# Kernel tuning notes

Hardware: AMD Instinct MI355X
Metric: run time of the kernel (lower is better)

Reference implementation:

```python
import jax, jax.numpy as jnp
import numpy as np


def setup_inputs() -> dict:
    key = jax.random.key(0)
    ks = jax.random.split(key, 5)
    B, C, H, W = 4, 256, 64, 64
    C8 = C // 8
    x = jax.random.normal(ks[0], (B, C, H, W), dtype=jnp.float32)
    # conv1x1 weights stored as [out, in] (kernel size 1 squeezed)
    wq = jax.random.normal(ks[1], (C8, C), dtype=jnp.float32) * (1.0 / np.sqrt(C))
    wk = jax.random.normal(ks[2], (C8, C), dtype=jnp.float32) * (1.0 / np.sqrt(C))
    wv = jax.random.normal(ks[3], (C, C), dtype=jnp.float32) * (1.0 / np.sqrt(C))
    bq = jnp.zeros((C8,), dtype=jnp.float32)
    bk = jnp.zeros((C8,), dtype=jnp.float32)
    bv = jnp.zeros((C,), dtype=jnp.float32)
    gamma = jax.random.normal(ks[4], (1,), dtype=jnp.float32)
    return {"x": x, "wq": wq, "bq": bq, "wk": wk, "bk": bk, "wv": wv, "bv": bv, "gamma": gamma}


def reference(x, wq, bq, wk, bk, wv, bv, gamma):
    B, C, H, W = x.shape
    flat = x.reshape(B, C, H * W)                      # [B, C, N]
    # 1x1 conv == channel matmul
    q = jnp.einsum('oc,bcn->bon', wq, flat) + bq[:, None]   # [B, C/8, N]
    k = jnp.einsum('oc,bcn->bon', wk, flat) + bk[:, None]   # [B, C/8, N]
    v = jnp.einsum('oc,bcn->bon', wv, flat) + bv[:, None]   # [B, C, N]
    # query permuted to [B, N, C/8]; scores [B, N, N]
    qk = jnp.einsum('bcn,bcm->bnm', q, k)
    # NOTE: softmax over dim=1 (over query index n), matching torch softmax(qk, 1)
    attn = jax.nn.softmax(qk, axis=1)
    out_attn = jnp.einsum('bcn,bnm->bcm', v, attn)     # [B, C, N]
    out = gamma[0] * out_attn.reshape(B, C, H, W) + x
    return out
```

## Files before the change

### kernel.cpp

```cpp
#include <hip/hip_runtime.h>

#define Bsz 4
#define Cch 256
#define Nsp 4096
#define XT_STRIDE 264

typedef _Float16 half8 __attribute__((ext_vector_type(8)));
typedef _Float16 half4v __attribute__((ext_vector_type(4)));
typedef short short8_t __attribute__((ext_vector_type(8)));
typedef float f32x4 __attribute__((ext_vector_type(4)));
typedef float fl4 __attribute__((ext_vector_type(4)));
typedef unsigned short ushort4v __attribute__((ext_vector_type(4)));

static __device__ __forceinline__ unsigned short f2bf(float f) {
  unsigned u = __builtin_bit_cast(unsigned, f);
  u += 0x7FFFu + ((u >> 16) & 1u);
  return (unsigned short)(u >> 16);
}

__global__ __launch_bounds__(256) void wconv_kernel(
    const float* __restrict__ wq, const float* __restrict__ wk, const float* __restrict__ wv,
    const float* __restrict__ bq, const float* __restrict__ bk, const float* __restrict__ bv,
    _Float16* __restrict__ Wh, float* __restrict__ bias)
{
  int t = blockIdx.x * 256 + threadIdx.x;
  int idx0 = t * 4;
  int o = idx0 >> 8, c = idx0 & 255;
  const float* src = (o < 32) ? (wq + o * 256)
                   : (o < 64) ? (wk + (o - 32) * 256)
                              : (wv + (o - 64) * 256);
  fl4 w4 = *(const fl4*)(src + c);
  half4v h;
#pragma unroll
  for (int j = 0; j < 4; ++j) h[j] = (_Float16)w4[j];
  *(half4v*)(Wh + idx0) = h;
  if (t < 320) bias[t] = (t < 32) ? bq[t] : (t < 64) ? bk[t - 32] : bv[t - 64];
}

__global__ __launch_bounds__(256) void proj_kernel(
    const float* __restrict__ x, const _Float16* __restrict__ Wh,
    const float* __restrict__ bias,
    _Float16* __restrict__ qh, _Float16* __restrict__ kh,
    unsigned short* __restrict__ vbuf)
{
  int bid = blockIdx.x;
  int nt  = bid & 127;
  int b   = bid >> 7;
  int n0  = nt * 32;
  int tid = threadIdx.x;
  int w   = tid >> 6, lane = tid & 63;
  int l15 = lane & 15, lg = lane >> 4;

  __shared__ __align__(16) _Float16 xT[32 * XT_STRIDE];

  const float* xb = x + (size_t)b * Cch * Nsp;

  {
    int n = lane & 31, ch = lane >> 5;
#pragma unroll
    for (int i = 0; i < 4; ++i) {
      int c0 = i * 64 + w * 16 + ch * 8;
      half8 hv;
#pragma unroll
      for (int j = 0; j < 8; ++j)
        hv[j] = (_Float16)xb[(size_t)(c0 + j) * Nsp + n0 + n];
      *(half8*)&xT[n * XT_STRIDE + c0] = hv;
    }
  }
  __syncthreads();

  int nsub = (w & 1) * 16;
  half8 bX[8];
#pragma unroll
  for (int k = 0; k < 8; ++k)
    bX[k] = *(const half8*)&xT[(nsub + l15) * XT_STRIDE + k * 32 + lg * 8];

  int n = n0 + nsub + l15;
  int ot0 = (w >> 1) * 10;
#pragma unroll
  for (int t = 0; t < 10; ++t) {
    int ot = ot0 + t;
    const _Float16* wrow = Wh + (size_t)(ot * 16 + l15) * 256 + lg * 8;
    f32x4 acc; acc[0]=0.f; acc[1]=0.f; acc[2]=0.f; acc[3]=0.f;
#pragma unroll
    for (int k = 0; k < 8; ++k) {
      half8 aW = *(const half8*)(wrow + k * 32);
      acc = __builtin_amdgcn_mfma_f32_16x16x32_f16(aW, bX[k], acc, 0, 0, 0);
    }
    fl4 bs = *(const fl4*)(bias + ot * 16 + lg * 4);
    if (ot < 2) {
      half4v qv;
#pragma unroll
      for (int r = 0; r < 4; ++r) qv[r] = (_Float16)(acc[r] + bs[r]);
      *(half4v*)(qh + ((size_t)b * Nsp + n) * 32 + ot * 16 + lg * 4) = qv;
    } else if (ot < 4) {
      half4v kv;
#pragma unroll
      for (int r = 0; r < 4; ++r) kv[r] = (_Float16)(acc[r] + bs[r]);
      *(half4v*)(kh + ((size_t)b * Nsp + n) * 32 + (ot - 2) * 16 + lg * 4) = kv;
    } else {
      int cv = (ot - 4) * 16 + lg * 4;
#pragma unroll
      for (int r = 0; r < 4; ++r)
        vbuf[((size_t)b * Cch + cv + r) * Nsp + n] = f2bf(acc[r] + bs[r]);
    }
  }
}

__global__ __launch_bounds__(1024) void attn_kernel(
    const _Float16* __restrict__ qh, const _Float16* __restrict__ kh,
    const unsigned short* __restrict__ vb, const float* __restrict__ x,
    const float* __restrict__ gamma, float* __restrict__ out)
{
  int bid  = blockIdx.x;
  int xcd  = bid & 7;
  int slot = bid >> 3;
  int b    = xcd >> 1;
  int mt   = slot + 32 * (xcd & 1);
  int m0   = mt * 64;
  int tid  = threadIdx.x;
  int w    = tid >> 6;
  int lane = tid & 63;
  int l15  = lane & 15, lg = lane >> 4;
  int wk   = w >> 3, wc = w & 7;

  __shared__ __align__(16) unsigned short P_lds[2][64][256];
  __shared__ float dpart[16][64];
  __shared__ float denom_s[64];

  const _Float16*       qb    = qh + (size_t)b * Nsp * 32;
  const _Float16*       kb    = kh + (size_t)b * Nsp * 32;
  const unsigned short* vbase = vb + (size_t)b * Cch * Nsp;

  half8 kB[4];
#pragma unroll
  for (int j = 0; j < 4; ++j)
    kB[j] = *(const half8*)(kb + (size_t)(m0 + 16 * j + l15) * 32 + lg * 8);

  f32x4 acc[2][4];
#pragma unroll
  for (int i = 0; i < 2; ++i)
#pragma unroll
    for (int j = 0; j < 4; ++j) { acc[i][j][0]=0.f; acc[i][j][1]=0.f; acc[i][j][2]=0.f; acc[i][j][3]=0.f; }

  float dsum[4] = {0.f, 0.f, 0.f, 0.f};

  const _Float16*       qp  = qb + (size_t)(16 * w + l15) * 32 + lg * 8;
  const unsigned short* pv0 = vbase + (size_t)(32 * wc + l15) * Nsp + 128 * wk + lg * 8;
  const unsigned short* pv1 = pv0 + (size_t)16 * Nsp;
  int xorh  = 8 * (l15 & 7);
  int wcol  = (16 * w + 4 * lg) ^ xorh;
  int rbase = 128 * wk + 8 * lg;

  half8 qA_a, qA_b;
  qA_a = *(const half8*)qp;

#define BODY(IT, BUF, QCUR, QNXT)                                              \
  {                                                                            \
    int n0 = (IT) * 256;                                                       \
    short8_t vf[4][2];  \
    _Pragma("unroll")                                                          \
    for (int k = 0; k < 4; ++k) {                                              \
      vf[k][0] = *(const short8_t*)(pv0 + n0 + 32 * k);                        \
      vf[k][1] = *(const short8_t*)(pv1 + n0 + 32 * k);                        \
    }                                                                          \
    f32x4 S[4];                                                                \
    _Pragma("unroll")                                                          \
    for (int j = 0; j < 4; ++j) {                                              \
      f32x4 z; z[0]=0.f; z[1]=0.f; z[2]=0.f; z[3]=0.f;                         \
      S[j] = __builtin_amdgcn_mfma_f32_16x16x32_f16(QCUR, kB[j], z, 0, 0, 0);  \
    }                                                                          \
    QNXT = *(const half8*)(qp + (size_t)(((IT) + 1) & 15) * 8192);             \
    ushort4v pb[4];                                                            \
    _Pragma("unroll")                                                          \
    for (int j = 0; j < 4; ++j) {                                              \
      _Pragma("unroll")                                                        \
      for (int r = 0; r < 4; ++r) {                                            \
        float p = __expf(S[j][r] - 20.0f);                                     \
        dsum[j] += p;                                                          \
        pb[j][r] = f2bf(p);                                                    \
      }                                                                        \
    }                                                                          \
    _Pragma("unroll")                                                          \
    for (int j = 0; j < 4; ++j)                                                \
      *(ushort4v*)&P_lds[BUF][16 * j + l15][wcol] = pb[j];                     \
    __syncthreads();                                                           \
    __builtin_amdgcn_s_setprio(1);                                             \
    _Pragma("unroll")                                                          \
    for (int k = 0; k < 4; ++k) {                                              \
      _Pragma("unroll")                                                        \
      for (int j = 0; j < 4; ++j) {                                            \
        int rc = (rbase + 32 * k) ^ xorh;                                      \
        short8_t bP = *(const short8_t*)&P_lds[BUF][16 * j + l15][rc];         \
        acc[0][j] = __builtin_amdgcn_mfma_f32_16x16x32_bf16(vf[k][0], bP, acc[0][j], 0, 0, 0); \
        acc[1][j] = __builtin_amdgcn_mfma_f32_16x16x32_bf16(vf[k][1], bP, acc[1][j], 0, 0, 0); \
      }                                                                        \
    }                                                                          \
    __builtin_amdgcn_s_setprio(0);                                             \
  }

  for (int it = 0; it < 16; it += 2) {
    BODY(it,     0, qA_a, qA_b)
    BODY(it + 1, 1, qA_b, qA_a)
  }
#undef BODY

#pragma unroll
  for (int j = 0; j < 4; ++j) {
    float d = dsum[j];
    d += __shfl_xor(d, 16);
    d += __shfl_xor(d, 32);
    dsum[j] = d;
  }
  if (lane < 16) {
#pragma unroll
    for (int j = 0; j < 4; ++j) dpart[w][16 * j + lane] = dsum[j];
  }
  __syncthreads();
  if (tid < 64) {
    float s = 0.f;
#pragma unroll
    for (int ww = 0; ww < 16; ++ww) s += dpart[ww][tid];
    denom_s[tid] = s;
  }
  float* mbuf = (float*)P_lds;
  if (w >= 8) {
#pragma unroll
    for (int c16 = 0; c16 < 2; ++c16)
#pragma unroll
      for (int j = 0; j < 4; ++j)
#pragma unroll
        for (int r = 0; r < 4; ++r)
          mbuf[lane + 64 * (((c16 * 4 + j) * 4 + r) + 32 * (w - 8))] = acc[c16][j][r];
  }
  __syncthreads();
  if (w < 8) {
    float g = gamma[0];
#pragma unroll
    for (int c16 = 0; c16 < 2; ++c16) {
#pragma unroll
      for (int j = 0; j < 4; ++j) {
        float dn = denom_s[16 * j + l15];
#pragma unroll
        for (int r = 0; r < 4; ++r) {
          float a = acc[c16][j][r] + mbuf[lane + 64 * (((c16 * 4 + j) * 4 + r) + 32 * w)];
          int c = 32 * w + 16 * c16 + 4 * lg + r;
          int m = m0 + 16 * j + l15;
          size_t idx = ((size_t)b * Cch + c) * Nsp + m;
          out[idx] = g * (a / dn) + x[idx];
        }
      }
    }
  }
}

extern "C" void kernel_launch(void* const* d_in, const int* in_sizes, int n_in,
                              void* d_out, int out_size, void* d_ws, size_t ws_size,
                              hipStream_t stream) {
  const float* x     = (const float*)d_in[0];
  const float* wq    = (const float*)d_in[1];
  const float* bq    = (const float*)d_in[2];
  const float* wk    = (const float*)d_in[3];
  const float* bk    = (const float*)d_in[4];
  const float* wv    = (const float*)d_in[5];
  const float* bv    = (const float*)d_in[6];
  const float* gamma = (const float*)d_in[7];
  float* out = (float*)d_out;

  char* ws = (char*)d_ws;
  _Float16*       qh   = (_Float16*)ws;
  _Float16*       kh   = (_Float16*)(ws + (1u << 20));
  unsigned short* vb   = (unsigned short*)(ws + (2u << 20));
  _Float16*       Wh   = (_Float16*)(ws + (10u << 20));
  float*          bias = (float*)(ws + (10u << 20) + (320u * 256u * 2u));

  wconv_kernel<<<dim3(80), dim3(256), 0, stream>>>(wq, wk, wv, bq, bk, bv, Wh, bias);
  proj_kernel<<<dim3(512), dim3(256), 0, stream>>>(x, Wh, bias, qh, kh, vb);
  attn_kernel<<<dim3(256), dim3(1024), 0, stream>>>(qh, kh, vb, x, gamma, out);
}
```

Measured before the change: 130.6 us.

## Software-pipeline QK softmax of next tile with PV MFMAs of current tile

Restructures the attention loop so the QK MFMA and exp/bf16 conversion for tile it+1 are interleaved with the PV MFMAs for tile it, writing P into the other LDS buffer, with a prologue and peeled epilogue. This reduces the exposed latency between score computation, the barrier and the PV matmul, leaving one barrier per iteration. It also replaces __expf(S-20) with exp2f of a fused multiply-add and pins waves_per_eu to 4. These raise register pressure, and the occupancy hint may cause spills.

Result: slower. 150.2 us (+15.1%).

```diff
diff --git a/kernel.cpp b/kernel.cpp
--- a/kernel.cpp
+++ b/kernel.cpp
@@ -11,6 +11,9 @@
 typedef float f32x4 __attribute__((ext_vector_type(4)));
 typedef float fl4 __attribute__((ext_vector_type(4)));
 typedef unsigned short ushort4v __attribute__((ext_vector_type(4)));
+
+#define LOG2E 1.4426950408889634f
+#define NSHIFT (-28.853900817779268f)
 
 static __device__ __forceinline__ unsigned short f2bf(float f) {
   unsigned u = __builtin_bit_cast(unsigned, f);
@@ -107,7 +110,8 @@
   }
 }
 
-__global__ __launch_bounds__(1024) void attn_kernel(
+__global__ __launch_bounds__(1024) __attribute__((amdgpu_waves_per_eu(4, 4)))
+void attn_kernel(
     const _Float16* __restrict__ qh, const _Float16* __restrict__ kh,
     const unsigned short* __restrict__ vb, const float* __restrict__ x,
     const float* __restrict__ gamma, float* __restrict__ out)
@@ -146,63 +150,86 @@
   float dsum[4] = {0.f, 0.f, 0.f, 0.f};
 
   const _Float16*       qp  = qb + (size_t)(16 * w + l15) * 32 + lg * 8;
+  const _Float16*       qn  = qp + 8192;
   const unsigned short* pv0 = vbase + (size_t)(32 * wc + l15) * Nsp + 128 * wk + lg * 8;
   const unsigned short* pv1 = pv0 + (size_t)16 * Nsp;
   int xorh  = 8 * (l15 & 7);
   int wcol  = (16 * w + 4 * lg) ^ xorh;
   int rbase = 128 * wk + 8 * lg;
 
-  half8 qA_a, qA_b;
-  qA_a = *(const half8*)qp;
-
-#define BODY(IT, BUF, QCUR, QNXT)                                              \
+  {
+    half8 qA0 = *(const half8*)qp;
+    ushort4v pb0[4];
+#pragma unroll
+    for (int j = 0; j < 4; ++j) {
+      f32x4 z; z[0]=0.f; z[1]=0.f; z[2]=0.f; z[3]=0.f;
+      f32x4 S0 = __builtin_amdgcn_mfma_f32_16x16x32_f16(qA0, kB[j], z, 0, 0, 0);
+#pragma unroll
+      for (int r = 0; r < 4; ++r) {
+        float p = exp2f(fmaf(S0[r], LOG2E, NSHIFT));
+        dsum[j] += p;
+        pb0[j][r] = f2bf(p);
+      }
+    }
+#pragma unroll
+    for (int j = 0; j < 4; ++j)
+      *(ushort4v*)&P_lds[0][16 * j + l15][wcol] = pb0[j];
+  }
+
+#define BODY(BUFC, BUFN, HN)                                                   \
   {                                                                            \
-    int n0 = (IT) * 256;                                                       \
-    short8_t vf[4][2];  \
+    __syncthreads();      \
+    half8 qA;                                                                  \
+    if (HN) qA = *(const half8*)qn;                                            \
+    short8_t vf[4][2];                                                         \
     _Pragma("unroll")                                                          \
     for (int k = 0; k < 4; ++k) {                                              \
-      vf[k][0] = *(const short8_t*)(pv0 + n0 + 32 * k);                        \
-      vf[k][1] = *(const short8_t*)(pv1 + n0 + 32 * k);                        \
+      vf[k][0] = *(const short8_t*)(pv0 + 32 * k);                             \
+      vf[k][1] = *(const short8_t*)(pv1 + 32 * k);                             \
     }                                                                          \
     f32x4 S[4];                                                                \
-    _Pragma("unroll")                                                          \
-    for (int j = 0; j < 4; ++j) {                                              \
-      f32x4 z; z[0]=0.f; z[1]=0.f; z[2]=0.f; z[3]=0.f;                         \
-      S[j] = __builtin_amdgcn_mfma_f32_16x16x32_f16(QCUR, kB[j], z, 0, 0, 0);  \
-    }                                                                          \
-    QNXT = *(const half8*)(qp + (size_t)(((IT) + 1) & 15) * 8192);             \
-    ushort4v pb[4];                                                            \
-    _Pragma("unroll")                                                          \
-    for (int j = 0; j < 4; ++j) {                                              \
+    if (HN) {                                                                  \
       _Pragma("unroll")                                                        \
-      for (int r = 0; r < 4; ++r) {                                            \
-        float p = __expf(S[j][r] - 20.0f);                                     \
-        dsum[j] += p;                                                          \
-        pb[j][r] = f2bf(p);                                                    \
+      for (int j = 0; j < 4; ++j) {                                            \
+        f32x4 z; z[0]=0.f; z[1]=0.f; z[2]=0.f; z[3]=0.f;                       \
+        S[j] = __builtin_amdgcn_mfma_f32_16x16x32_f16(qA, kB[j], z, 0, 0, 0);  \
       }                                                                        \
     }                                                                          \
-    _Pragma("unroll")                                                          \
-    for (int j = 0; j < 4; ++j)                                                \
-      *(ushort4v*)&P_lds[BUF][16 * j + l15][wcol] = pb[j];                     \
-    __syncthreads();                                                           \
+    ushort4v pb[4];                                                            \
     __builtin_amdgcn_s_setprio(1);                                             \
     _Pragma("unroll")                                                          \
     for (int k = 0; k < 4; ++k) {                                              \
       _Pragma("unroll")                                                        \
       for (int j = 0; j < 4; ++j) {                                            \
         int rc = (rbase + 32 * k) ^ xorh;                                      \
-        short8_t bP = *(const short8_t*)&P_lds[BUF][16 * j + l15][rc];         \
+        short8_t bP = *(const short8_t*)&P_lds[BUFC][16 * j + l15][rc];        \
         acc[0][j] = __builtin_amdgcn_mfma_f32_16x16x32_bf16(vf[k][0], bP, acc[0][j], 0, 0, 0); \
         acc[1][j] = __builtin_amdgcn_mfma_f32_16x16x32_bf16(vf[k][1], bP, acc[1][j], 0, 0, 0); \
       }                                                                        \
+      if (HN) {        \
+        _Pragma("unroll")                                                      \
+        for (int r = 0; r < 4; ++r) {                                          \
+          float p = exp2f(fmaf(S[k][r], LOG2E, NSHIFT));                       \
+          dsum[k] += p;                                                        \
+          pb[k][r] = f2bf(p);                                                  \
+        }                                                                      \
+      }                                                                        \
     }                                                                          \
     __builtin_amdgcn_s_setprio(0);                                             \
-  }
-
-  for (int it = 0; it < 16; it += 2) {
-    BODY(it,     0, qA_a, qA_b)
-    BODY(it + 1, 1, qA_b, qA_a)
-  }
+    if (HN) {                                                                  \
+      _Pragma("unroll")                                                        \
+      for (int j = 0; j < 4; ++j)                                              \
+        *(ushort4v*)&P_lds[BUFN][16 * j + l15][wcol] = pb[j];                  \
+    }                                                                          \
+    pv0 += 256; pv1 += 256; qn += 8192;                                        \
+  }
+
+  for (int it = 0; it < 7; ++it) {
+    BODY(0, 1, true)
+    BODY(1, 0, true)
+  }
+  BODY(0, 1, true)
+  BODY(1, 0, false)
 #undef BODY
 
 #pragma unroll
```
